# Kernel optimization log

Measured on AMD Instinct MI355X. Metric: run time of the kernel, lower is better.

## Reference

```python
import jax, jax.numpy as jnp
import numpy as np

B, N, DIM = 4, 4096, 128
DEG, EXP = 2, 2
DE = DEG * EXP * DIM  # 512, expanded projection dim


def setup_inputs() -> dict:
    key = jax.random.key(0)
    ks = jax.random.split(key, 7)
    xq = jax.random.normal(ks[0], (B, N, DIM), dtype=jnp.float32)
    # causal 3D mask (batch, query_len, context_len)
    mask = jnp.broadcast_to(jnp.tril(jnp.ones((N, N), jnp.float32)), (B, N, N))
    sc_in = 1.0 / np.sqrt(DIM)
    sc_de = 1.0 / np.sqrt(DE)
    W_se = jax.random.normal(ks[1], (DE, DIM), jnp.float32) * sc_in
    b_se = jax.random.normal(ks[2], (DE,), jnp.float32) * 0.01
    W_po = jax.random.normal(ks[3], (DE, DIM), jnp.float32) * sc_in
    b_po = jax.random.normal(ks[4], (DE,), jnp.float32) * 0.01
    W_ag = jax.random.normal(ks[5], (DIM, DE), jnp.float32) * sc_de
    b_ag = jax.random.normal(ks[6], (DIM,), jnp.float32) * 0.01
    return {"xq": xq, "mask": mask, "W_se": W_se, "b_se": b_se,
            "W_po": W_po, "b_po": b_po, "W_ag": W_ag, "b_ag": b_ag}


def reference(xq, mask, W_se, b_se, W_po, b_po, W_ag, b_ag):
    # self-attention: xc = xq
    s = xq @ W_se.T + b_se                       # [B, N, DE]
    h = xq @ W_po.T + b_po                       # [B, N, DE]
    # po2: second-order polynomial expansion (exact-erf GELU, torch default)
    g = jax.nn.gelu(h, approximate=False)
    h1, h2 = jnp.split(g, 2, axis=-1)
    h = jnp.concatenate([h1, h2 * h1], axis=-1)  # [B, N, DE]
    # full_mask_mixer: masked aggregation + normalization
    agg = jnp.einsum('bnd,bmn->bmd', h, mask)    # [B, M, DE]
    agg = agg / (1e-7 + jnp.sum(mask, axis=2, keepdims=True))
    # polynomial selection: sigmoid gating
    o = jax.nn.sigmoid(s) * agg                  # [B, N, DE]
    return o @ W_ag.T + b_ag                     # [B, N, DIM]
```

## Files before the change

kernel.cpp:

```cpp
#include <hip/hip_runtime.h>
#include <math.h>

#define BB 4
#define NN 4096
#define DIM 128
#define DE 512
#define NTOK (BB * NN)
#define CH 32
#define NCHUNK (NN / CH)

typedef __attribute__((ext_vector_type(8))) short bf16x8;
typedef __attribute__((ext_vector_type(4))) float f32x4;
typedef unsigned short us;

__device__ inline us f2bf(float f) {
    union { float f; unsigned int u; } v; v.f = f;
    unsigned int r = v.u + 0x7FFF + ((v.u >> 16) & 1);
    return (us)(r >> 16);
}
__device__ inline float bf2f(unsigned int h16) {
    union { unsigned int u; float f; } v; v.u = (h16 & 0xFFFFu) << 16;
    return v.f;
}
__device__ inline float gelu_erf(float x) {
    return 0.5f * x * (1.0f + erff(x * 0.70710678118654752f));
}
__device__ inline float sigmoidf(float x) {
    return 1.0f / (1.0f + expf(-x));
}

__global__ __launch_bounds__(256) void k0_pack(
    const float* __restrict__ Wse, const float* __restrict__ Wpo,
    const float* __restrict__ Wag, us* __restrict__ wp)
{
    int gid = blockIdx.x * 256 + threadIdx.x;
    int mat = gid >> 13;
    int r   = gid & 8191;
    int f   = r >> 6;
    int lane = r & 63;
    const float* src = (mat == 0) ? Wse : ((mat == 1) ? Wpo : Wag);
    int K     = (mat == 2) ? DE : DIM;
    int shift = (mat == 2) ? 4 : 2;
    int ct = f >> shift;
    int ks = f & ((1 << shift) - 1);
    int col = ct * 16 + (lane & 15);
    int k0  = ks * 32 + (lane >> 4) * 8;
    const float* s = &src[(size_t)col * K + k0];
    float4 a = *(const float4*)s;
    float4 b = *(const float4*)(s + 4);
    us o[8] = { f2bf(a.x), f2bf(a.y), f2bf(a.z), f2bf(a.w),
                f2bf(b.x), f2bf(b.y), f2bf(b.z), f2bf(b.w) };
    us* d = wp + (size_t)mat * 65536 + ((size_t)f * 64 + lane) * 8;
    *(ushort4*)d       = *(ushort4*)&o[0];
    *(ushort4*)(d + 4) = *(ushort4*)&o[4];
}

#define XPAD 8
__global__ __launch_bounds__(256) void k1_hsum(
    const float* __restrict__ xq, const us* __restrict__ wpo,
    const float* __restrict__ b_po, us* __restrict__ hp,
    float* __restrict__ S)
{
    __shared__ us xs[CH][DIM + XPAD];
    __shared__ float Ssum[DE];

    const int tid = threadIdx.x;
    const int blk = blockIdx.x;
    const size_t t0 = (size_t)blk * CH;

    Ssum[tid] = 0.f;
    Ssum[tid + 256] = 0.f;

    for (int i = tid * 4; i < CH * DIM; i += 1024) {
        int tok = i >> 7, k = i & 127;
        float4 v = *(const float4*)&xq[(t0 + tok) * DIM + k];
        ushort4 o = { f2bf(v.x), f2bf(v.y), f2bf(v.z), f2bf(v.w) };
        *(ushort4*)&xs[tok][k] = o;
    }
    __syncthreads();

    const int lane = tid & 63, w = tid >> 6;
    const int tg = w & 1, chf = w >> 1;
    const int l15 = lane & 15, q = lane >> 4;

    bf16x8 af[4];
    #pragma unroll
    for (int ks = 0; ks < 4; ++ks)
        af[ks] = *(const bf16x8*)&xs[tg * 16 + l15][ks * 32 + q * 8];

    f32x4 accL[8], accH[8];
    #pragma unroll
    for (int i = 0; i < 8; ++i) {
        accL[i] = (f32x4){0.f, 0.f, 0.f, 0.f};
        accH[i] = (f32x4){0.f, 0.f, 0.f, 0.f};
    }

    #pragma unroll
    for (int ks = 0; ks < 4; ++ks) {
        #pragma unroll
        for (int i = 0; i < 8; ++i) {
            int ctL = chf * 8 + i;
            bf16x8 bL = *(const bf16x8*)&wpo[(size_t)((ctL * 4 + ks) * 64 + lane) * 8];
            bf16x8 bH = *(const bf16x8*)&wpo[(size_t)(((ctL + 16) * 4 + ks) * 64 + lane) * 8];
            accL[i] = __builtin_amdgcn_mfma_f32_16x16x32_bf16(af[ks], bL, accL[i], 0, 0, 0);
            accH[i] = __builtin_amdgcn_mfma_f32_16x16x32_bf16(af[ks], bH, accH[i], 0, 0, 0);
        }
    }

    #pragma unroll
    for (int i = 0; i < 8; ++i) {
        int colL = (chf * 8 + i) * 16 + l15;
        int colH = colL + 256;
        float bL = b_po[colL], bH = b_po[colH];
        float g1v[4], h2v[4];
        float sL = 0.f, sH = 0.f;
        #pragma unroll
        for (int r = 0; r < 4; ++r) {
            float g1 = gelu_erf(accL[i][r] + bL);
            float g2 = gelu_erf(accH[i][r] + bH);
            g1v[r] = g1;
            h2v[r] = g2 * g1;
            sL += g1;
            sH += h2v[r];
        }
        uint4 st;
        st.x = (unsigned)f2bf(g1v[0]) | ((unsigned)f2bf(g1v[1]) << 16);
        st.y = (unsigned)f2bf(g1v[2]) | ((unsigned)f2bf(g1v[3]) << 16);
        st.z = (unsigned)f2bf(h2v[0]) | ((unsigned)f2bf(h2v[1]) << 16);
        st.w = (unsigned)f2bf(h2v[2]) | ((unsigned)f2bf(h2v[3]) << 16);
        *(uint4*)&hp[((((size_t)blk * 4 + w) * 8 + i) * 64 + lane) * 8] = st;

        sL += __shfl_xor(sL, 16); sL += __shfl_xor(sL, 32);
        sH += __shfl_xor(sH, 16); sH += __shfl_xor(sH, 32);
        if (q == 0) {
            atomicAdd(&Ssum[colL], sL);
            atomicAdd(&Ssum[colH], sH);
        }
    }
    __syncthreads();
    S[(size_t)blk * DE + tid]       = Ssum[tid];
    S[(size_t)blk * DE + tid + 256] = Ssum[tid + 256];
}

#define OPAD 8
__global__ __launch_bounds__(256) void k3_fused(
    const float* __restrict__ xq, const us* __restrict__ hp,
    const us* __restrict__ wse, const us* __restrict__ wag,
    const float* __restrict__ b_se, const float* __restrict__ S,
    const float* __restrict__ b_ag, float* __restrict__ out)
{
    __shared__ us xs[CH][DIM + XPAD];
    __shared__ us ht[CH][DE + OPAD];
    __shared__ float pre[DE];

    const int tid = threadIdx.x;
    const int blk = blockIdx.x;
    const int c = blk & (NCHUNK - 1);
    const int b = blk >> 7;
    const size_t t0 = (size_t)blk * CH;

    const int lane = tid & 63, w = tid >> 6;
    const int tg = w & 1, chf = w >> 1;
    const int l15 = lane & 15, q = lane >> 4;

    uint4 hv[8];
    #pragma unroll
    for (int i = 0; i < 8; ++i)
        hv[i] = *(const uint4*)&hp[((((size_t)blk * 4 + w) * 8 + i) * 64 + lane) * 8];

    for (int i = tid * 4; i < CH * DIM; i += 1024) {
        int tok = i >> 7, k = i & 127;
        float4 v = *(const float4*)&xq[(t0 + tok) * DIM + k];
        ushort4 o = { f2bf(v.x), f2bf(v.y), f2bf(v.z), f2bf(v.w) };
        *(ushort4*)&xs[tok][k] = o;
    }

    {
        int d = tid * 2;
        float r0 = 0.f, r1 = 0.f;
        const float* p = &S[((size_t)b * NCHUNK) * DE + d];
        for (int cc = 0; cc < c; ++cc) {
            float2 v = *(const float2*)p;
            r0 += v.x; r1 += v.y;
            p += DE;
        }
        pre[d] = r0; pre[d + 1] = r1;
    }

    #pragma unroll
    for (int i = 0; i < 8; ++i) {
        int colL = (chf * 8 + i) * 16 + l15;
        int colH = colL + 256;
        int tokb = tg * 16 + q * 4;
        ht[tokb + 0][colL] = (us)(hv[i].x);
        ht[tokb + 1][colL] = (us)(hv[i].x >> 16);
        ht[tokb + 2][colL] = (us)(hv[i].y);
        ht[tokb + 3][colL] = (us)(hv[i].y >> 16);
        ht[tokb + 0][colH] = (us)(hv[i].z);
        ht[tokb + 1][colH] = (us)(hv[i].z >> 16);
        ht[tokb + 2][colH] = (us)(hv[i].w);
        ht[tokb + 3][colH] = (us)(hv[i].w >> 16);
    }
    __syncthreads();

    {
        int d = tid * 2;
        float r0 = pre[d], r1 = pre[d + 1];
        #pragma unroll 4
        for (int n = 0; n < CH; ++n) {
            unsigned hvv = *(unsigned*)&ht[n][d];
            r0 += bf2f(hvv);
            r1 += bf2f(hvv >> 16);
            float inv = 1.0f / ((float)(c * CH + n + 1) + 1e-7f);
            *(unsigned*)&ht[n][d] = (unsigned)f2bf(r0 * inv)
                                  | ((unsigned)f2bf(r1 * inv) << 16);
        }
    }
    __syncthreads();

    bf16x8 af[4];
    #pragma unroll
    for (int ks = 0; ks < 4; ++ks)
        af[ks] = *(const bf16x8*)&xs[tg * 16 + l15][ks * 32 + q * 8];

    {
        f32x4 accL[8], accH[8];
        #pragma unroll
        for (int i = 0; i < 8; ++i) {
            accL[i] = (f32x4){0.f, 0.f, 0.f, 0.f};
            accH[i] = (f32x4){0.f, 0.f, 0.f, 0.f};
        }
        #pragma unroll
        for (int ks = 0; ks < 4; ++ks) {
            #pragma unroll
            for (int i = 0; i < 8; ++i) {
                int ctL = chf * 8 + i;
                bf16x8 bL = *(const bf16x8*)&wse[(size_t)((ctL * 4 + ks) * 64 + lane) * 8];
                bf16x8 bH = *(const bf16x8*)&wse[(size_t)(((ctL + 16) * 4 + ks) * 64 + lane) * 8];
                accL[i] = __builtin_amdgcn_mfma_f32_16x16x32_bf16(af[ks], bL, accL[i], 0, 0, 0);
                accH[i] = __builtin_amdgcn_mfma_f32_16x16x32_bf16(af[ks], bH, accH[i], 0, 0, 0);
            }
        }
        #pragma unroll
        for (int i = 0; i < 8; ++i) {
            int colL = (chf * 8 + i) * 16 + l15;
            int colH = colL + 256;
            float bL = b_se[colL], bH = b_se[colH];
            #pragma unroll
            for (int r = 0; r < 4; ++r) {
                int tok = tg * 16 + q * 4 + r;
                float aggL = bf2f((unsigned)ht[tok][colL]);
                float aggH = bf2f((unsigned)ht[tok][colH]);
                ht[tok][colL] = f2bf(sigmoidf(accL[i][r] + bL) * aggL);
                ht[tok][colH] = f2bf(sigmoidf(accH[i][r] + bH) * aggH);
            }
        }
    }
    __syncthreads();

    {
        f32x4 acc[4];
        #pragma unroll
        for (int i = 0; i < 4; ++i) acc[i] = (f32x4){0.f, 0.f, 0.f, 0.f};

        for (int ks = 0; ks < 16; ++ks) {
            bf16x8 a = *(const bf16x8*)&ht[tg * 16 + l15][ks * 32 + q * 8];
            #pragma unroll
            for (int i = 0; i < 4; ++i) {
                int ct = chf * 4 + i;
                bf16x8 bb = *(const bf16x8*)&wag[(size_t)((ct * 16 + ks) * 64 + lane) * 8];
                acc[i] = __builtin_amdgcn_mfma_f32_16x16x32_bf16(a, bb, acc[i], 0, 0, 0);
            }
        }
        #pragma unroll
        for (int i = 0; i < 4; ++i) {
            int col = (chf * 4 + i) * 16 + l15;
            float bv = b_ag[col];
            #pragma unroll
            for (int r = 0; r < 4; ++r) {
                size_t tok = t0 + tg * 16 + q * 4 + r;
                out[tok * DIM + col] = acc[i][r] + bv;
            }
        }
    }
}

extern "C" void kernel_launch(void* const* d_in, const int* in_sizes, int n_in,
                              void* d_out, int out_size, void* d_ws, size_t ws_size,
                              hipStream_t stream)
{
    const float* xq   = (const float*)d_in[0];
    const float* W_se = (const float*)d_in[2];
    const float* b_se = (const float*)d_in[3];
    const float* W_po = (const float*)d_in[4];
    const float* b_po = (const float*)d_in[5];
    const float* W_ag = (const float*)d_in[6];
    const float* b_ag = (const float*)d_in[7];
    float* out = (float*)d_out;

    us* wp  = (us*)d_ws;
    us* wse = wp;
    us* wpo = wp + 65536;
    us* wag = wp + 131072;
    float* S = (float*)(wp + 196608);
    us* hp   = (us*)(S + (size_t)BB * NCHUNK * DE);

    k0_pack<<<96, 256, 0, stream>>>(W_se, W_po, W_ag, wp);
    k1_hsum<<<NTOK / CH, 256, 0, stream>>>(xq, wpo, b_po, hp, S);
    k3_fused<<<NTOK / CH, 256, 0, stream>>>(xq, hp, wse, wag, b_se, S, b_ag, out);
}
```

Measured before the change: 385.9 us.

## Add chunk-prefix scan kernel, register-level cumsum, fast erf/exp, direct x loads

Adds a separate scan kernel that turns per-chunk column sums into exclusive prefixes, so the gate kernel no longer re-reads up to 127 prior chunk sums per block (quadratic work). The in-chunk cumulative sum moves from a serial shared-memory loop to register prefix sums with wave shuffles, and x is loaded straight into MFMA fragments instead of being staged in LDS. It also swaps exact erff/expf for a polynomial erf approximation and __expf, which trades some accuracy for cheaper transcendentals. The cost is one extra small kernel launch whose grid of 4 blocks runs serially over 128 chunks.

```diff
diff --git a/kernel.cpp b/kernel.cpp
--- a/kernel.cpp
+++ b/kernel.cpp
@@ -8,6 +8,7 @@
 #define NTOK (BB * NN)
 #define CH 32
 #define NCHUNK (NN / CH)
+#define NBLK (NTOK / CH)
 
 typedef __attribute__((ext_vector_type(8))) short bf16x8;
 typedef __attribute__((ext_vector_type(4))) float f32x4;
@@ -22,11 +23,19 @@
     union { unsigned int u; float f; } v; v.u = (h16 & 0xFFFFu) << 16;
     return v.f;
 }
+__device__ inline float erf_fast(float x) {
+    float ax = fabsf(x);
+    float t = 1.0f / (1.0f + 0.3275911f * ax);
+    float poly = t * (0.254829592f + t * (-0.284496736f +
+                 t * (1.421413741f + t * (-1.453152027f + t * 1.061405429f))));
+    float r = 1.0f - poly * __expf(-ax * ax);
+    return copysignf(r, x);
+}
 __device__ inline float gelu_erf(float x) {
-    return 0.5f * x * (1.0f + erff(x * 0.70710678118654752f));
+    return 0.5f * x * (1.0f + erf_fast(x * 0.70710678118654752f));
 }
 __device__ inline float sigmoidf(float x) {
-    return 1.0f / (1.0f + expf(-x));
+    return 1.0f / (1.0f + __expf(-x));
 }
 
 __global__ __launch_bounds__(256) void k0_pack(
@@ -55,13 +64,11 @@
     *(ushort4*)(d + 4) = *(ushort4*)&o[4];
 }
 
-#define XPAD 8
 __global__ __launch_bounds__(256) void k1_hsum(
     const float* __restrict__ xq, const us* __restrict__ wpo,
     const float* __restrict__ b_po, us* __restrict__ hp,
     float* __restrict__ S)
 {
-    __shared__ us xs[CH][DIM + XPAD];
     __shared__ float Ssum[DE];
 
     const int tid = threadIdx.x;
@@ -71,22 +78,22 @@
     Ssum[tid] = 0.f;
     Ssum[tid + 256] = 0.f;
 
-    for (int i = tid * 4; i < CH * DIM; i += 1024) {
-        int tok = i >> 7, k = i & 127;
-        float4 v = *(const float4*)&xq[(t0 + tok) * DIM + k];
-        ushort4 o = { f2bf(v.x), f2bf(v.y), f2bf(v.z), f2bf(v.w) };
-        *(ushort4*)&xs[tok][k] = o;
-    }
-    __syncthreads();
-
     const int lane = tid & 63, w = tid >> 6;
     const int tg = w & 1, chf = w >> 1;
     const int l15 = lane & 15, q = lane >> 4;
 
     bf16x8 af[4];
-    #pragma unroll
-    for (int ks = 0; ks < 4; ++ks)
-        af[ks] = *(const bf16x8*)&xs[tg * 16 + l15][ks * 32 + q * 8];
+    {
+        const float* xrow = xq + (t0 + tg * 16 + l15) * DIM;
+        #pragma unroll
+        for (int ks = 0; ks < 4; ++ks) {
+            float4 a0 = *(const float4*)&xrow[ks * 32 + q * 8];
+            float4 a1 = *(const float4*)&xrow[ks * 32 + q * 8 + 4];
+            us t[8] = { f2bf(a0.x), f2bf(a0.y), f2bf(a0.z), f2bf(a0.w),
+                        f2bf(a1.x), f2bf(a1.y), f2bf(a1.z), f2bf(a1.w) };
+            af[ks] = *(bf16x8*)t;
+        }
+    }
 
     f32x4 accL[8], accH[8];
     #pragma unroll
@@ -94,7 +101,6 @@
         accL[i] = (f32x4){0.f, 0.f, 0.f, 0.f};
         accH[i] = (f32x4){0.f, 0.f, 0.f, 0.f};
     }
-
     #pragma unroll
     for (int ks = 0; ks < 4; ++ks) {
         #pragma unroll
@@ -106,6 +112,8 @@
             accH[i] = __builtin_amdgcn_mfma_f32_16x16x32_bf16(af[ks], bH, accH[i], 0, 0, 0);
         }
     }
+
+    __syncthreads();
 
     #pragma unroll
     for (int i = 0; i < 8; ++i) {
@@ -142,21 +150,39 @@
     S[(size_t)blk * DE + tid + 256] = Ssum[tid + 256];
 }
 
+__global__ __launch_bounds__(256) void k2s_scan(float* __restrict__ S)
+{
+    const int b = blockIdx.x;
+    const int d0 = threadIdx.x * 2;
+    float r0 = 0.f, r1 = 0.f;
+    for (int g = 0; g < NCHUNK / 8; ++g) {
+        float2 v[8];
+        #pragma unroll
+        for (int j = 0; j < 8; ++j)
+            v[j] = *(const float2*)&S[((size_t)b * NCHUNK + g * 8 + j) * DE + d0];
+        #pragma unroll
+        for (int j = 0; j < 8; ++j) {
+            float2 e = { r0, r1 };
+            *(float2*)&S[((size_t)b * NCHUNK + g * 8 + j) * DE + d0] = e;
+            r0 += v[j].x; r1 += v[j].y;
+        }
+    }
+}
+
 #define OPAD 8
-__global__ __launch_bounds__(256) void k3_fused(
+__global__ __launch_bounds__(256) void k3_gate_out(
     const float* __restrict__ xq, const us* __restrict__ hp,
     const us* __restrict__ wse, const us* __restrict__ wag,
     const float* __restrict__ b_se, const float* __restrict__ S,
     const float* __restrict__ b_ag, float* __restrict__ out)
 {
-    __shared__ us xs[CH][DIM + XPAD];
     __shared__ us ht[CH][DE + OPAD];
     __shared__ float pre[DE];
+    __shared__ float halfT[DE];
 
     const int tid = threadIdx.x;
     const int blk = blockIdx.x;
     const int c = blk & (NCHUNK - 1);
-    const int b = blk >> 7;
     const size_t t0 = (size_t)blk * CH;
 
     const int lane = tid & 63, w = tid >> 6;
@@ -168,61 +194,25 @@
     for (int i = 0; i < 8; ++i)
         hv[i] = *(const uint4*)&hp[((((size_t)blk * 4 + w) * 8 + i) * 64 + lane) * 8];
 
-    for (int i = tid * 4; i < CH * DIM; i += 1024) {
-        int tok = i >> 7, k = i & 127;
-        float4 v = *(const float4*)&xq[(t0 + tok) * DIM + k];
-        ushort4 o = { f2bf(v.x), f2bf(v.y), f2bf(v.z), f2bf(v.w) };
-        *(ushort4*)&xs[tok][k] = o;
-    }
-
-    {
-        int d = tid * 2;
-        float r0 = 0.f, r1 = 0.f;
-        const float* p = &S[((size_t)b * NCHUNK) * DE + d];
-        for (int cc = 0; cc < c; ++cc) {
-            float2 v = *(const float2*)p;
-            r0 += v.x; r1 += v.y;
-            p += DE;
-        }
-        pre[d] = r0; pre[d + 1] = r1;
-    }
-
-    #pragma unroll
-    for (int i = 0; i < 8; ++i) {
-        int colL = (chf * 8 + i) * 16 + l15;
-        int colH = colL + 256;
-        int tokb = tg * 16 + q * 4;
-        ht[tokb + 0][colL] = (us)(hv[i].x);
-        ht[tokb + 1][colL] = (us)(hv[i].x >> 16);
-        ht[tokb + 2][colL] = (us)(hv[i].y);
-        ht[tokb + 3][colL] = (us)(hv[i].y >> 16);
-        ht[tokb + 0][colH] = (us)(hv[i].z);
-        ht[tokb + 1][colH] = (us)(hv[i].z >> 16);
-        ht[tokb + 2][colH] = (us)(hv[i].w);
-        ht[tokb + 3][colH] = (us)(hv[i].w >> 16);
-    }
-    __syncthreads();
-
-    {
-        int d = tid * 2;
-        float r0 = pre[d], r1 = pre[d + 1];
-        #pragma unroll 4
-        for (int n = 0; n < CH; ++n) {
-            unsigned hvv = *(unsigned*)&ht[n][d];
-            r0 += bf2f(hvv);
-            r1 += bf2f(hvv >> 16);
-            float inv = 1.0f / ((float)(c * CH + n + 1) + 1e-7f);
-            *(unsigned*)&ht[n][d] = (unsigned)f2bf(r0 * inv)
-                                  | ((unsigned)f2bf(r1 * inv) << 16);
-        }
-    }
-    __syncthreads();
+    {
+        float2 p = *(const float2*)&S[(size_t)blk * DE + tid * 2];
+        *(float2*)&pre[tid * 2] = p;
+    }
 
     bf16x8 af[4];
-    #pragma unroll
-    for (int ks = 0; ks < 4; ++ks)
-        af[ks] = *(const bf16x8*)&xs[tg * 16 + l15][ks * 32 + q * 8];
-
+    {
+        const float* xrow = xq + (t0 + tg * 16 + l15) * DIM;
+        #pragma unroll
+        for (int ks = 0; ks < 4; ++ks) {
+            float4 a0 = *(const float4*)&xrow[ks * 32 + q * 8];
+            float4 a1 = *(const float4*)&xrow[ks * 32 + q * 8 + 4];
+            us t[8] = { f2bf(a0.x), f2bf(a0.y), f2bf(a0.z), f2bf(a0.w),
+                        f2bf(a1.x), f2bf(a1.y), f2bf(a1.z), f2bf(a1.w) };
+            af[ks] = *(bf16x8*)t;
+        }
+    }
+
+    uint4 sgv[8];
     {
         f32x4 accL[8], accH[8];
         #pragma unroll
@@ -244,16 +234,67 @@
         #pragma unroll
         for (int i = 0; i < 8; ++i) {
             int colL = (chf * 8 + i) * 16 + l15;
-            int colH = colL + 256;
-            float bL = b_se[colL], bH = b_se[colH];
+            float bL = b_se[colL], bH = b_se[colL + 256];
+            us sl[4], sh[4];
             #pragma unroll
             for (int r = 0; r < 4; ++r) {
-                int tok = tg * 16 + q * 4 + r;
-                float aggL = bf2f((unsigned)ht[tok][colL]);
-                float aggH = bf2f((unsigned)ht[tok][colH]);
-                ht[tok][colL] = f2bf(sigmoidf(accL[i][r] + bL) * aggL);
-                ht[tok][colH] = f2bf(sigmoidf(accH[i][r] + bH) * aggH);
+                sl[r] = f2bf(sigmoidf(accL[i][r] + bL));
+                sh[r] = f2bf(sigmoidf(accH[i][r] + bH));
             }
+            sgv[i].x = (unsigned)sl[0] | ((unsigned)sl[1] << 16);
+            sgv[i].y = (unsigned)sl[2] | ((unsigned)sl[3] << 16);
+            sgv[i].z = (unsigned)sh[0] | ((unsigned)sh[1] << 16);
+            sgv[i].w = (unsigned)sh[2] | ((unsigned)sh[3] << 16);
+        }
+    }
+
+    float pL[8][4], pH[8][4];
+    float qexL[8], qexH[8];
+    #pragma unroll
+    for (int i = 0; i < 8; ++i) {
+        float v0 = bf2f(hv[i].x), v1 = bf2f(hv[i].x >> 16);
+        float v2 = bf2f(hv[i].y), v3 = bf2f(hv[i].y >> 16);
+        pL[i][0] = v0; pL[i][1] = v0 + v1;
+        pL[i][2] = pL[i][1] + v2; pL[i][3] = pL[i][2] + v3;
+        float u0 = bf2f(hv[i].z), u1 = bf2f(hv[i].z >> 16);
+        float u2 = bf2f(hv[i].w), u3 = bf2f(hv[i].w >> 16);
+        pH[i][0] = u0; pH[i][1] = u0 + u1;
+        pH[i][2] = pH[i][1] + u2; pH[i][3] = pH[i][2] + u3;
+
+        float scL = pL[i][3];
+        float uu = __shfl_up(scL, 16); scL += (q >= 1) ? uu : 0.f;
+        uu = __shfl_up(scL, 32);       scL += (q >= 2) ? uu : 0.f;
+        float scH = pH[i][3];
+        uu = __shfl_up(scH, 16);       scH += (q >= 1) ? uu : 0.f;
+        uu = __shfl_up(scH, 32);       scH += (q >= 2) ? uu : 0.f;
+        qexL[i] = scL - pL[i][3];
+        qexH[i] = scH - pH[i][3];
+
+        float htL = __shfl(scL, l15 + 48);
+        float htH = __shfl(scH, l15 + 48);
+        if (tg == 0 && q == 0) {
+            int colL = (chf * 8 + i) * 16 + l15;
+            halfT[colL] = htL;
+            halfT[colL + 256] = htH;
+        }
+    }
+    __syncthreads();
+
+    #pragma unroll
+    for (int i = 0; i < 8; ++i) {
+        int colL = (chf * 8 + i) * 16 + l15;
+        int colH = colL + 256;
+        float baseL = pre[colL] + qexL[i] + (tg ? halfT[colL] : 0.f);
+        float baseH = pre[colH] + qexH[i] + (tg ? halfT[colH] : 0.f);
+        unsigned sgp[4] = { sgv[i].x, sgv[i].y, sgv[i].z, sgv[i].w };
+        #pragma unroll
+        for (int r = 0; r < 4; ++r) {
+            int tok = tg * 16 + q * 4 + r;
+            float inv = 1.0f / ((float)(c * CH + tok + 1) + 1e-7f);
+            float sL = bf2f(r & 1 ? sgp[r >> 1] >> 16 : sgp[r >> 1]);
+            float sH = bf2f(r & 1 ? sgp[2 + (r >> 1)] >> 16 : sgp[2 + (r >> 1)]);
+            ht[tok][colL] = f2bf(sL * (baseL + pL[i][r]) * inv);
+            ht[tok][colH] = f2bf(sH * (baseH + pH[i][r]) * inv);
         }
     }
     __syncthreads();
@@ -303,9 +344,10 @@
     us* wpo = wp + 65536;
     us* wag = wp + 131072;
     float* S = (float*)(wp + 196608);
-    us* hp   = (us*)(S + (size_t)BB * NCHUNK * DE);
+    us* hp   = (us*)(S + (size_t)NBLK * DE);
 
     k0_pack<<<96, 256, 0, stream>>>(W_se, W_po, W_ag, wp);
-    k1_hsum<<<NTOK / CH, 256, 0, stream>>>(xq, wpo, b_po, hp, S);
-    k3_fused<<<NTOK / CH, 256, 0, stream>>>(xq, hp, wse, wag, b_se, S, b_ag, out);
-}
+    k1_hsum<<<NBLK, 256, 0, stream>>>(xq, wpo, b_po, hp, S);
+    k2s_scan<<<BB, 256, 0, stream>>>(S);
+    k3_gate_out<<<NBLK, 256, 0, stream>>>(xq, hp, wse, wag, b_se, S, b_ag, out);
+}
```

Result: faster. 357.3 us (-7.4%).
